# Kernel tuning notes

Hardware: AMD Instinct MI355X
Metric: run time of the kernel (lower is better)

Reference implementation:

```python
import jax, jax.numpy as jnp
import numpy as np

NUM_EXPERTS = 8
HIDDEN = 1024
TOKENS = 8192


def setup_inputs() -> dict:
    key = jax.random.key(0)
    k1, k2, k3, k4 = jax.random.split(key, 4)
    inp = jax.random.normal(k1, (TOKENS, HIDDEN), dtype=jnp.float32)
    gate = jax.random.normal(k2, (TOKENS, NUM_EXPERTS), dtype=jnp.float32)
    # expert parameters: one dense layer per expert (H -> H)
    W = jax.random.normal(k3, (NUM_EXPERTS, HIDDEN, HIDDEN), dtype=jnp.float32) / np.sqrt(HIDDEN)
    b = jax.random.normal(k4, (NUM_EXPERTS, HIDDEN), dtype=jnp.float32) * 0.01
    return {"input": inp, "gate": gate, "W": W, "b": b}


def reference(input, gate, W, b):
    # Routing: softmax over router logits, top-1 expert per token.
    probs = jax.nn.softmax(gate, axis=-1)            # [T, E]
    expert_idx = jnp.argmax(probs, axis=-1)          # [T]
    top_p = jnp.take_along_axis(probs, expert_idx[:, None], axis=-1)[:, 0]  # [T]

    # Dispatch + grouped GEMM (computed densely for all experts, then masked):
    # y[e, t, d] = input[t, :] @ W[e] + b[e]
    y = jnp.einsum("th,ehd->etd", input, W) + b[:, None, :]  # [E, T, H]

    # Combine: select the routed expert's output, scaled by its gate prob.
    dispatch = jax.nn.one_hot(expert_idx, NUM_EXPERTS, dtype=input.dtype) * top_p[:, None]  # [T, E]
    out = jnp.einsum("etd,te->td", y, dispatch)      # [T, H]
    return out
```

## Files before the change

kernel.cpp:

```cpp
#include <hip/hip_runtime.h>
#include <hip/hip_bf16.h>
#include <cstdint>
#include <cstddef>

#define TOK 8192
#define HID 1024
#define NE 8

typedef __bf16 bf16x4 __attribute__((ext_vector_type(4)));
typedef __bf16 bf16x8 __attribute__((ext_vector_type(8)));
typedef float floatx4 __attribute__((ext_vector_type(4)));

static __device__ __forceinline__ __bf16 f2bf(float x) {
    unsigned u = __builtin_bit_cast(unsigned, x);
    u += 0x7fffu + ((u >> 16) & 1u);
    unsigned short hs = (unsigned short)(u >> 16);
    return __builtin_bit_cast(__bf16, hs);
}

__global__ void prep_kernel(const float* __restrict__ X, const float* __restrict__ gate,
                            const float* __restrict__ W,
                            __bf16* __restrict__ Xb, __bf16* __restrict__ Wt,
                            float* __restrict__ scale, int* __restrict__ counts,
                            int* __restrict__ list) {
    const int b = blockIdx.x;
    const int t = threadIdx.x;

    if (b < 1024) {
        const int e  = b >> 7;
        const int rem = b & 127;
        const int kt = rem >> 4;
        const int nt = rem & 15;
        const int k0 = kt * 128, n0 = nt * 64;
        const int cg = t & 15;
        const int rg = t >> 4;

        const float* src = W + ((size_t)e * HID + k0 + rg * 8) * HID + n0 + cg * 4;
        float rr[8][4];
#pragma unroll
        for (int i = 0; i < 8; i++) {
            float4 x = *(const float4*)(src + (size_t)i * HID);
            rr[i][0] = x.x; rr[i][1] = x.y; rr[i][2] = x.z; rr[i][3] = x.w;
        }
        __bf16* dst = Wt + ((size_t)e * HID + n0 + cg * 4) * HID + k0 + rg * 8;
#pragma unroll
        for (int j = 0; j < 4; j++) {
            bf16x8 v;
#pragma unroll
            for (int i = 0; i < 8; i++) v[i] = f2bf(rr[i][j]);
            *(bf16x8*)(dst + (size_t)j * HID) = v;
        }
    } else {
        const int bb = b - 1024;
        size_t idx = (size_t)bb * 256 + t;
        const float4 a0 = *(const float4*)(X + idx * 8);
        const float4 a1 = *(const float4*)(X + idx * 8 + 4);
        bf16x8 v;
        v[0] = f2bf(a0.x); v[1] = f2bf(a0.y); v[2] = f2bf(a0.z); v[3] = f2bf(a0.w);
        v[4] = f2bf(a1.x); v[5] = f2bf(a1.y); v[6] = f2bf(a1.z); v[7] = f2bf(a1.w);
        *(bf16x8*)(Xb + idx * 8) = v;

        if (bb < 32) {
            __shared__ int hcnt[NE];
            __shared__ int hbase[NE];
            if (t < NE) hcnt[t] = 0;
            __syncthreads();
            int tok = bb * 256 + t;
            float g[NE];
#pragma unroll
            for (int j = 0; j < NE; j++) g[j] = gate[tok * NE + j];
            float gm = g[0]; int best = 0;
#pragma unroll
            for (int j = 1; j < NE; j++) {
                if (g[j] > gm) { gm = g[j]; best = j; }
            }
            float s = 0.f;
#pragma unroll
            for (int j = 0; j < NE; j++) s += __expf(g[j] - gm);
            scale[tok] = 1.0f / s;
            int lpos = atomicAdd(&hcnt[best], 1);
            __syncthreads();
            if (t < NE) hbase[t] = atomicAdd(&counts[t], hcnt[t]);
            __syncthreads();
            list[best * TOK + hbase[best] + lpos] = tok;
        }
    }
}

__launch_bounds__(256)
__global__ void moe_gemm_bf16(const __bf16* __restrict__ Xb, const __bf16* __restrict__ Wt,
                              const float* __restrict__ Bias, const float* __restrict__ scale,
                              const int* __restrict__ counts, const int* __restrict__ list,
                              float* __restrict__ out) {
    const int bid = blockIdx.x;
    const int e  = bid & 7;
    const int nt = (bid >> 3) & 15;
    const int mt = bid >> 7;

    const int cnt = counts[e];
    if (mt * 64 >= cnt) return;
    const int mvalid = min(64, cnt - mt * 64);
    const int n0 = nt * 64;

    __shared__ __bf16 As[3][64 * 64];
    __shared__ __bf16 Bs[3][64 * 64];
    __shared__ int   tok[64];
    __shared__ float scl[64];

    const int tid  = threadIdx.x;
    const int lane = tid & 63;
    const int wave = tid >> 6;

    if (tid < 64) {
        int g = mt * 64 + tid;
        int tk = (g < cnt) ? list[e * TOK + g] : 0;
        tok[tid] = tk;
        scl[tid] = (g < cnt) ? scale[tk] : 0.f;
    }
    __syncthreads();

    const int srow = lane >> 3;
    const int gchunk = ((lane & 7) ^ srow) * 8;
    const __bf16* aptr[2];
    const __bf16* bptr[2];
#pragma unroll
    for (int i = 0; i < 2; i++) {
        int r = wave * 16 + i * 8 + srow;
        aptr[i] = Xb + (size_t)tok[r] * HID + gchunk;
        bptr[i] = Wt + ((size_t)e * HID + n0 + r) * HID + gchunk;
    }

    const int ln = lane & 15;
    const int q  = lane >> 4;
    const int wm = (wave >> 1) * 32;
    const int wn = (wave & 1) * 32;
    const int rsw = ln & 7;

    floatx4 acc[2][2];
#pragma unroll
    for (int mi = 0; mi < 2; mi++)
#pragma unroll
        for (int ni = 0; ni < 2; ni++) acc[mi][ni] = (floatx4){0.f, 0.f, 0.f, 0.f};

    auto stage = [&](int b, int k0) {
#pragma unroll
        for (int i = 0; i < 2; i++) {
            __builtin_amdgcn_global_load_lds(
                (const __attribute__((address_space(1))) void*)(aptr[i] + k0),
                (__attribute__((address_space(3))) void*)(&As[b][(wave * 16 + i * 8) * 64]),
                16, 0, 0);
            __builtin_amdgcn_global_load_lds(
                (const __attribute__((address_space(1))) void*)(bptr[i] + k0),
                (__attribute__((address_space(3))) void*)(&Bs[b][(wave * 16 + i * 8) * 64]),
                16, 0, 0);
        }
    };

    auto compute = [&](int b) {
        __builtin_amdgcn_s_setprio(1);
#pragma unroll
        for (int kk = 0; kk < 64; kk += 32) {
            const int cb = (kk >> 3) + q;
            const int pos = (cb ^ rsw) * 8;
            bf16x8 af[2], bfv[2];
#pragma unroll
            for (int mi = 0; mi < 2; mi++)
                af[mi] = *(const bf16x8*)(&As[b][(wm + mi * 16 + ln) * 64 + pos]);
#pragma unroll
            for (int ni = 0; ni < 2; ni++)
                bfv[ni] = *(const bf16x8*)(&Bs[b][(wn + ni * 16 + ln) * 64 + pos]);
#pragma unroll
            for (int mi = 0; mi < 2; mi++)
#pragma unroll
                for (int ni = 0; ni < 2; ni++)
                    acc[mi][ni] = __builtin_amdgcn_mfma_f32_16x16x32_bf16(
                        af[mi], bfv[ni], acc[mi][ni], 0, 0, 0);
        }
        __builtin_amdgcn_s_setprio(0);
    };

    stage(0, 0);
    stage(1, 64);

#pragma unroll
    for (int t = 0; t < 14; ++t) {
        __builtin_amdgcn_s_barrier();
        stage((t + 2) % 3, (t + 2) * 64);
        asm volatile("s_waitcnt vmcnt(8)" ::: "memory");
        __builtin_amdgcn_s_barrier();
        compute(t % 3);
    }
    asm volatile("s_waitcnt vmcnt(4)" ::: "memory");
    __builtin_amdgcn_s_barrier();
    compute(14 % 3);
    asm volatile("s_waitcnt vmcnt(0)" ::: "memory");
    __builtin_amdgcn_s_barrier();
    compute(15 % 3);

    float bn[2];
#pragma unroll
    for (int ni = 0; ni < 2; ni++) bn[ni] = Bias[e * HID + n0 + wn + ni * 16 + ln];

#pragma unroll
    for (int mi = 0; mi < 2; mi++) {
#pragma unroll
        for (int r = 0; r < 4; r++) {
            int row = wm + mi * 16 + q * 4 + r;
            if (row < mvalid) {
                int t = tok[row];
                float sc = scl[row];
                size_t ob = (size_t)t * HID + n0 + wn + ln;
#pragma unroll
                for (int ni = 0; ni < 2; ni++)
                    __builtin_nontemporal_store(sc * (acc[mi][ni][r] + bn[ni]),
                                                &out[ob + ni * 16]);
            }
        }
    }
}

__launch_bounds__(256)
__global__ void moe_gemm_fb(const float* __restrict__ X, const float* __restrict__ W,
                            const float* __restrict__ Bias, const float* __restrict__ scale,
                            const int* __restrict__ counts, const int* __restrict__ list,
                            float* __restrict__ out) {
    const int bid = blockIdx.x;
    const int e  = bid >> 9;
    const int nt = (bid >> 6) & 7;
    const int mt = bid & 63;
    const int cnt = counts[e];
    if (mt * 128 >= cnt) return;
    const int mvalid = min(128, cnt - mt * 128);
    const int n0 = nt * 128;

    __shared__ __bf16 As[128 * 64];
    __shared__ __bf16 Bs[128 * 64];
    __shared__ int   tok[128];
    __shared__ float scl[128];

    const int tid = threadIdx.x;
    if (tid < 128) {
        int g = mt * 128 + tid;
        int tk = (g < cnt) ? list[e * TOK + g] : 0;
        tok[tid] = tk;
        scl[tid] = (g < cnt) ? scale[tk] : 0.f;
    }
    __syncthreads();

    const int c4 = tid & 15;
    const float* rp[8];
    bool rv[8];
#pragma unroll
    for (int i = 0; i < 8; i++) {
        int m = (tid >> 4) + 16 * i;
        rv[i] = (m < mvalid);
        rp[i] = X + (size_t)tok[m] * HID;
    }
    const int n4 = tid & 31;
    const int kb = tid >> 5;
    const float* wbase = W + (size_t)e * HID * HID + (size_t)(kb * 8) * HID + n0 + n4 * 4;

    const int lane = tid & 63;
    const int ln = lane & 15;
    const int q  = lane >> 4;
    const int wave = tid >> 6;
    const int wm = (wave >> 1) * 64;
    const int wn = (wave & 1) * 64;

    floatx4 acc[4][4];
#pragma unroll
    for (int mi = 0; mi < 4; mi++)
#pragma unroll
        for (int ni = 0; ni < 4; ni++) acc[mi][ni] = (floatx4){0.f, 0.f, 0.f, 0.f};

    for (int k0 = 0; k0 < HID; k0 += 64) {
#pragma unroll
        for (int i = 0; i < 8; i++) {
            int m = (tid >> 4) + 16 * i;
            float4 v = make_float4(0.f, 0.f, 0.f, 0.f);
            if (rv[i]) v = *(const float4*)(rp[i] + k0 + c4 * 4);
            bf16x4 b4;
            b4[0] = f2bf(v.x); b4[1] = f2bf(v.y); b4[2] = f2bf(v.z); b4[3] = f2bf(v.w);
            int chunk = c4 >> 1;
            int addr = m * 64 + ((chunk ^ (m & 7)) * 8) + (c4 & 1) * 4;
            *(bf16x4*)(&As[addr]) = b4;
        }
        {
            const float* wp = wbase + (size_t)k0 * HID;
            float4 rr[8];
#pragma unroll
            for (int r = 0; r < 8; r++) rr[r] = *(const float4*)(wp + (size_t)r * HID);
#pragma unroll
            for (int j = 0; j < 4; j++) {
                int n = n4 * 4 + j;
                int c = kb ^ (n & 7);
                bf16x8 pk;
                pk[0] = f2bf(j == 0 ? rr[0].x : j == 1 ? rr[0].y : j == 2 ? rr[0].z : rr[0].w);
                pk[1] = f2bf(j == 0 ? rr[1].x : j == 1 ? rr[1].y : j == 2 ? rr[1].z : rr[1].w);
                pk[2] = f2bf(j == 0 ? rr[2].x : j == 1 ? rr[2].y : j == 2 ? rr[2].z : rr[2].w);
                pk[3] = f2bf(j == 0 ? rr[3].x : j == 1 ? rr[3].y : j == 2 ? rr[3].z : rr[3].w);
                pk[4] = f2bf(j == 0 ? rr[4].x : j == 1 ? rr[4].y : j == 2 ? rr[4].z : rr[4].w);
                pk[5] = f2bf(j == 0 ? rr[5].x : j == 1 ? rr[5].y : j == 2 ? rr[5].z : rr[5].w);
                pk[6] = f2bf(j == 0 ? rr[6].x : j == 1 ? rr[6].y : j == 2 ? rr[6].z : rr[6].w);
                pk[7] = f2bf(j == 0 ? rr[7].x : j == 1 ? rr[7].y : j == 2 ? rr[7].z : rr[7].w);
                *(bf16x8*)(&Bs[n * 64 + c * 8]) = pk;
            }
        }
        __syncthreads();
#pragma unroll
        for (int kk = 0; kk < 64; kk += 32) {
            const int cbase = (kk >> 3) + q;
            bf16x8 af[4], bfv[4];
#pragma unroll
            for (int mi = 0; mi < 4; mi++) {
                int row = wm + mi * 16 + ln;
                af[mi] = *(const bf16x8*)(&As[row * 64 + ((cbase ^ (row & 7)) * 8)]);
            }
#pragma unroll
            for (int ni = 0; ni < 4; ni++) {
                int n = wn + ni * 16 + ln;
                bfv[ni] = *(const bf16x8*)(&Bs[n * 64 + ((cbase ^ (n & 7)) * 8)]);
            }
#pragma unroll
            for (int mi = 0; mi < 4; mi++)
#pragma unroll
                for (int ni = 0; ni < 4; ni++)
                    acc[mi][ni] = __builtin_amdgcn_mfma_f32_16x16x32_bf16(
                        af[mi], bfv[ni], acc[mi][ni], 0, 0, 0);
        }
        __syncthreads();
    }

    float bn[4];
#pragma unroll
    for (int ni = 0; ni < 4; ni++) bn[ni] = Bias[e * HID + n0 + wn + ni * 16 + ln];
#pragma unroll
    for (int mi = 0; mi < 4; mi++) {
#pragma unroll
        for (int r = 0; r < 4; r++) {
            int row = wm + mi * 16 + q * 4 + r;
            if (row < mvalid) {
                int t = tok[row];
                float sc = scl[row];
                size_t ob = (size_t)t * HID + n0 + wn + ln;
#pragma unroll
                for (int ni = 0; ni < 4; ni++)
                    out[ob + ni * 16] = sc * (acc[mi][ni][r] + bn[ni]);
            }
        }
    }
}

__global__ void route_fb_kernel(const float* __restrict__ gate, float* __restrict__ scale,
                                int* __restrict__ counts, int* __restrict__ list) {
    int t = blockIdx.x * blockDim.x + threadIdx.x;
    if (t >= TOK) return;
    float g[NE];
#pragma unroll
    for (int j = 0; j < NE; j++) g[j] = gate[t * NE + j];
    float gm = g[0]; int best = 0;
#pragma unroll
    for (int j = 1; j < NE; j++) {
        if (g[j] > gm) { gm = g[j]; best = j; }
    }
    float s = 0.f;
#pragma unroll
    for (int j = 0; j < NE; j++) s += __expf(g[j] - gm);
    scale[t] = 1.0f / s;
    int pos = atomicAdd(&counts[best], 1);
    list[best * TOK + pos] = t;
}

extern "C" void kernel_launch(void* const* d_in, const int* in_sizes, int n_in,
                              void* d_out, int out_size, void* d_ws, size_t ws_size,
                              hipStream_t stream) {
    const float* X    = (const float*)d_in[0];
    const float* G    = (const float*)d_in[1];
    const float* W    = (const float*)d_in[2];
    const float* Bias = (const float*)d_in[3];
    float* out = (float*)d_out;

    float* scale = (float*)d_ws;
    int* counts  = (int*)((char*)d_ws + 32768);
    int* list    = (int*)((char*)d_ws + 36864);
    __bf16* Xb   = (__bf16*)((char*)d_ws + 299008);
    __bf16* Wt   = (__bf16*)((char*)d_ws + 299008 + 16777216);
    const size_t need = 299008 + 2 * 16777216ULL;

    hipMemsetAsync(counts, 0, NE * sizeof(int), stream);

    if (ws_size >= need) {
        prep_kernel<<<5120, 256, 0, stream>>>(X, G, W, Xb, Wt, scale, counts, list);
        moe_gemm_bf16<<<128 * 16 * 8, 256, 0, stream>>>(Xb, Wt, Bias, scale, counts, list, out);
    } else {
        route_fb_kernel<<<TOK / 256, 256, 0, stream>>>(G, scale, counts, list);
        moe_gemm_fb<<<NE * 64 * 8, 256, 0, stream>>>(X, W, Bias, scale, counts, list, out);
    }
}
```

Measured before the change: 142.0 us.

## Fuse prep and grouped GEMM into one cooperative persistent kernel with grid sync

Replaces the separate prep (weight transpose/convert, input convert, routing) and grouped-GEMM launches with a single cooperative kernel of 512 persistent blocks. A grid-wide sync separates the two phases, and the GEMM tiles are processed in a grid-stride loop. The aim is to remove one kernel launch and its tail/launch gap. In exchange, parallelism drops from thousands of blocks to a fixed 512, and the grid-sync barrier adds cost. If the cooperative launch fails, it falls back to the old two-kernel path.

New measurement: 242.0 us. 1.7x slower.

```diff
diff --git a/kernel.cpp b/kernel.cpp
--- a/kernel.cpp
+++ b/kernel.cpp
@@ -1,11 +1,15 @@
 #include <hip/hip_runtime.h>
 #include <hip/hip_bf16.h>
+#include <hip/hip_cooperative_groups.h>
 #include <cstdint>
 #include <cstddef>
+
+namespace cg = cooperative_groups;
 
 #define TOK 8192
 #define HID 1024
 #define NE 8
+#define FGRID 512
 
 typedef __bf16 bf16x4 __attribute__((ext_vector_type(4)));
 typedef __bf16 bf16x8 __attribute__((ext_vector_type(8)));
@@ -16,6 +20,207 @@
     u += 0x7fffu + ((u >> 16) & 1u);
     unsigned short hs = (unsigned short)(u >> 16);
     return __builtin_bit_cast(__bf16, hs);
+}
+
+__launch_bounds__(256)
+__global__ void fused_moe(const float* __restrict__ X, const float* __restrict__ gate,
+                          const float* __restrict__ W,
+                          __bf16* __restrict__ Xb, __bf16* __restrict__ Wt,
+                          const float* __restrict__ Bias,
+                          float* __restrict__ scale, int* __restrict__ counts,
+                          int* __restrict__ list, float* __restrict__ out) {
+    __shared__ __bf16 As[3][64 * 64];
+    __shared__ __bf16 Bs[3][64 * 64];
+    __shared__ int   tok[64];
+    __shared__ float scl[64];
+    __shared__ int hcnt[NE];
+    __shared__ int hbase[NE];
+
+    const int bid = blockIdx.x;
+    const int tid = threadIdx.x;
+
+    for (int u = bid; u < 1024; u += FGRID) {
+        const int e  = u >> 7;
+        const int rem = u & 127;
+        const int kt = rem >> 4;
+        const int nt = rem & 15;
+        const int k0 = kt * 128, n0 = nt * 64;
+        const int cg_ = tid & 15;
+        const int rg = tid >> 4;
+
+        const float* src = W + ((size_t)e * HID + k0 + rg * 8) * HID + n0 + cg_ * 4;
+        float rr[8][4];
+#pragma unroll
+        for (int i = 0; i < 8; i++) {
+            float4 x = *(const float4*)(src + (size_t)i * HID);
+            rr[i][0] = x.x; rr[i][1] = x.y; rr[i][2] = x.z; rr[i][3] = x.w;
+        }
+        __bf16* dst = Wt + ((size_t)e * HID + n0 + cg_ * 4) * HID + k0 + rg * 8;
+#pragma unroll
+        for (int j = 0; j < 4; j++) {
+            bf16x8 v;
+#pragma unroll
+            for (int i = 0; i < 8; i++) v[i] = f2bf(rr[i][j]);
+            *(bf16x8*)(dst + (size_t)j * HID) = v;
+        }
+    }
+
+#pragma unroll
+    for (int it = 0; it < 8; ++it) {
+        size_t idx = (size_t)it * (FGRID * 256) + bid * 256 + tid;
+        const float4 a0 = *(const float4*)(X + idx * 8);
+        const float4 a1 = *(const float4*)(X + idx * 8 + 4);
+        bf16x8 v;
+        v[0] = f2bf(a0.x); v[1] = f2bf(a0.y); v[2] = f2bf(a0.z); v[3] = f2bf(a0.w);
+        v[4] = f2bf(a1.x); v[5] = f2bf(a1.y); v[6] = f2bf(a1.z); v[7] = f2bf(a1.w);
+        *(bf16x8*)(Xb + idx * 8) = v;
+    }
+
+    if (bid < 32) {
+        if (tid < NE) hcnt[tid] = 0;
+        __syncthreads();
+        int tk = bid * 256 + tid;
+        float g[NE];
+#pragma unroll
+        for (int j = 0; j < NE; j++) g[j] = gate[tk * NE + j];
+        float gm = g[0]; int best = 0;
+#pragma unroll
+        for (int j = 1; j < NE; j++) {
+            if (g[j] > gm) { gm = g[j]; best = j; }
+        }
+        float s = 0.f;
+#pragma unroll
+        for (int j = 0; j < NE; j++) s += __expf(g[j] - gm);
+        scale[tk] = 1.0f / s;
+        int lpos = atomicAdd(&hcnt[best], 1);
+        __syncthreads();
+        if (tid < NE) hbase[tid] = atomicAdd(&counts[tid], hcnt[tid]);
+        __syncthreads();
+        list[best * TOK + hbase[best] + lpos] = tk;
+    }
+
+    cg::this_grid().sync();
+
+    const int lane = tid & 63;
+    const int wave = tid >> 6;
+    const int ln = lane & 15;
+    const int q  = lane >> 4;
+    const int wm = (wave >> 1) * 32;
+    const int wn = (wave & 1) * 32;
+    const int rsw = ln & 7;
+    const int srow = lane >> 3;
+    const int gchunk = ((lane & 7) ^ srow) * 8;
+
+    for (int w = bid; w < 128 * 16 * 8; w += FGRID) {
+        const int e  = w & 7;
+        const int nt = (w >> 3) & 15;
+        const int mt = w >> 7;
+
+        const int cnt = counts[e];
+        if (mt * 64 >= cnt) continue;
+        const int mvalid = min(64, cnt - mt * 64);
+        const int n0 = nt * 64;
+
+        __syncthreads();
+        if (tid < 64) {
+            int g = mt * 64 + tid;
+            int tk = (g < cnt) ? list[e * TOK + g] : 0;
+            tok[tid] = tk;
+            scl[tid] = (g < cnt) ? scale[tk] : 0.f;
+        }
+        __syncthreads();
+
+        const __bf16* aptr[2];
+        const __bf16* bptr[2];
+#pragma unroll
+        for (int i = 0; i < 2; i++) {
+            int r = wave * 16 + i * 8 + srow;
+            aptr[i] = Xb + (size_t)tok[r] * HID + gchunk;
+            bptr[i] = Wt + ((size_t)e * HID + n0 + r) * HID + gchunk;
+        }
+
+        floatx4 acc[2][2];
+#pragma unroll
+        for (int mi = 0; mi < 2; mi++)
+#pragma unroll
+            for (int ni = 0; ni < 2; ni++) acc[mi][ni] = (floatx4){0.f, 0.f, 0.f, 0.f};
+
+        auto stage = [&](int b, int k0) {
+#pragma unroll
+            for (int i = 0; i < 2; i++) {
+                __builtin_amdgcn_global_load_lds(
+                    (const __attribute__((address_space(1))) void*)(aptr[i] + k0),
+                    (__attribute__((address_space(3))) void*)(&As[b][(wave * 16 + i * 8) * 64]),
+                    16, 0, 0);
+                __builtin_amdgcn_global_load_lds(
+                    (const __attribute__((address_space(1))) void*)(bptr[i] + k0),
+                    (__attribute__((address_space(3))) void*)(&Bs[b][(wave * 16 + i * 8) * 64]),
+                    16, 0, 0);
+            }
+        };
+
+        auto compute = [&](int b) {
+            __builtin_amdgcn_s_setprio(1);
+#pragma unroll
+            for (int kk = 0; kk < 64; kk += 32) {
+                const int cb = (kk >> 3) + q;
+                const int pos = (cb ^ rsw) * 8;
+                bf16x8 af[2], bfv[2];
+#pragma unroll
+                for (int mi = 0; mi < 2; mi++)
+                    af[mi] = *(const bf16x8*)(&As[b][(wm + mi * 16 + ln) * 64 + pos]);
+#pragma unroll
+                for (int ni = 0; ni < 2; ni++)
+                    bfv[ni] = *(const bf16x8*)(&Bs[b][(wn + ni * 16 + ln) * 64 + pos]);
+#pragma unroll
+                for (int mi = 0; mi < 2; mi++)
+#pragma unroll
+                    for (int ni = 0; ni < 2; ni++)
+                        acc[mi][ni] = __builtin_amdgcn_mfma_f32_16x16x32_bf16(
+                            af[mi], bfv[ni], acc[mi][ni], 0, 0, 0);
+            }
+            __builtin_amdgcn_s_setprio(0);
+        };
+
+        stage(0, 0);
+        stage(1, 64);
+
+#pragma unroll
+        for (int t = 0; t < 14; ++t) {
+            __builtin_amdgcn_s_barrier();
+            stage((t + 2) % 3, (t + 2) * 64);
+            asm volatile("s_waitcnt vmcnt(8)" ::: "memory");
+            __builtin_amdgcn_s_barrier();
+            compute(t % 3);
+        }
+        asm volatile("s_waitcnt vmcnt(4)" ::: "memory");
+        __builtin_amdgcn_s_barrier();
+        compute(14 % 3);
+        asm volatile("s_waitcnt vmcnt(0)" ::: "memory");
+        __builtin_amdgcn_s_barrier();
+        compute(15 % 3);
+
+        float bn[2];
+#pragma unroll
+        for (int ni = 0; ni < 2; ni++) bn[ni] = Bias[e * HID + n0 + wn + ni * 16 + ln];
+
+#pragma unroll
+        for (int mi = 0; mi < 2; mi++) {
+#pragma unroll
+            for (int r = 0; r < 4; r++) {
+                int row = wm + mi * 16 + q * 4 + r;
+                if (row < mvalid) {
+                    int t = tok[row];
+                    float sc = scl[row];
+                    size_t ob = (size_t)t * HID + n0 + wn + ln;
+#pragma unroll
+                    for (int ni = 0; ni < 2; ni++)
+                        __builtin_nontemporal_store(sc * (acc[mi][ni][r] + bn[ni]),
+                                                    &out[ob + ni * 16]);
+                }
+            }
+        }
+    }
 }
 
 __global__ void prep_kernel(const float* __restrict__ X, const float* __restrict__ gate,
@@ -32,17 +237,17 @@
         const int kt = rem >> 4;
         const int nt = rem & 15;
         const int k0 = kt * 128, n0 = nt * 64;
-        const int cg = t & 15;
+        const int cg_ = t & 15;
         const int rg = t >> 4;
 
-        const float* src = W + ((size_t)e * HID + k0 + rg * 8) * HID + n0 + cg * 4;
+        const float* src = W + ((size_t)e * HID + k0 + rg * 8) * HID + n0 + cg_ * 4;
         float rr[8][4];
 #pragma unroll
         for (int i = 0; i < 8; i++) {
             float4 x = *(const float4*)(src + (size_t)i * HID);
             rr[i][0] = x.x; rr[i][1] = x.y; rr[i][2] = x.z; rr[i][3] = x.w;
         }
-        __bf16* dst = Wt + ((size_t)e * HID + n0 + cg * 4) * HID + k0 + rg * 8;
+        __bf16* dst = Wt + ((size_t)e * HID + n0 + cg_ * 4) * HID + k0 + rg * 8;
 #pragma unroll
         for (int j = 0; j < 4; j++) {
             bf16x8 v;
@@ -390,8 +595,16 @@
     hipMemsetAsync(counts, 0, NE * sizeof(int), stream);
 
     if (ws_size >= need) {
-        prep_kernel<<<5120, 256, 0, stream>>>(X, G, W, Xb, Wt, scale, counts, list);
-        moe_gemm_bf16<<<128 * 16 * 8, 256, 0, stream>>>(Xb, Wt, Bias, scale, counts, list, out);
+        void* args[] = {(void*)&X, (void*)&G, (void*)&W, (void*)&Xb, (void*)&Wt,
+                        (void*)&Bias, (void*)&scale, (void*)&counts, (void*)&list,
+                        (void*)&out};
+        hipError_t err = hipLaunchCooperativeKernel(
+            (const void*)fused_moe, dim3(FGRID), dim3(256), args, 0, stream);
+        if (err != hipSuccess) {
+            prep_kernel<<<5120, 256, 0, stream>>>(X, G, W, Xb, Wt, scale, counts, list);
+            moe_gemm_bf16<<<128 * 16 * 8, 256, 0, stream>>>(Xb, Wt, Bias, scale, counts,
+                                                            list, out);
+        }
     } else {
         route_fb_kernel<<<TOK / 256, 256, 0, stream>>>(G, scale, counts, list);
         moe_gemm_fb<<<NE * 64 * 8, 256, 0, stream>>>(X, W, Bias, scale, counts, list, out);
```
